# Kernel tuning notes

Measured on AMD Instinct MI355X. Metric: run time of the kernel, lower is better.

The kernel has to match this reference:

```python
import jax, jax.numpy as jnp
import numpy as np
from jax import lax

DIM = 256
HEADS = 8
C3 = DIM * 3 // 4  # 192
C1 = DIM // 4      # 64


def conv1x1(x, w):
    # x: [b,c,h,w], w: [o,c] (1x1 conv, no bias)
    return jnp.einsum('bchw,oc->bohw', x, w)


def dwconv3x3(x, w):
    # x: [b,c,h,w], w: [c,1,3,3] depthwise
    return lax.conv_general_dilated(
        x, w, window_strides=(1, 1), padding='SAME',
        feature_group_count=x.shape[1],
        dimension_numbers=('NCHW', 'OIHW', 'NCHW'))


def l2norm(x, eps=1e-12):
    # torch F.normalize: x / max(||x||, eps) along last dim
    n = jnp.sqrt(jnp.sum(x * x, axis=-1, keepdims=True))
    return x / jnp.maximum(n, eps)


def setup_inputs() -> dict:
    key = jax.random.key(0)
    ks = jax.random.split(key, 10)
    s = 0.02
    return {
        'x': jax.random.normal(ks[0], (4, DIM, 128, 128), jnp.float32),
        'k_v': jax.random.normal(ks[1], (4, 256), jnp.float32),
        'temperature': jnp.ones((HEADS, 1, 1), jnp.float32),
        'w_kR': jax.random.normal(ks[2], (C3, 192), jnp.float32) * s,
        'w_kI': jax.random.normal(ks[3], (C1, 64), jnp.float32) * s,
        'w_qR': jax.random.normal(ks[4], (DIM, C3), jnp.float32) * s,
        'w_qdw': jax.random.normal(ks[5], (DIM, 1, 3, 3), jnp.float32) * s,
        'w_kvI': jax.random.normal(ks[6], (2 * DIM, C1), jnp.float32) * s,
        'w_kvdw': jax.random.normal(ks[7], (2 * DIM, 1, 3, 3), jnp.float32) * s,
        'w_proj': jax.random.normal(ks[8], (DIM, DIM), jnp.float32) * s,
    }


def reference(x, k_v, temperature, w_kR, w_kI, w_qR, w_qdw, w_kvI, w_kvdw, w_proj):
    b, c, h, w = x.shape
    # FiLM-style modulation: x * kv + x
    kvr = (k_v[:, :192] @ w_kR.T)[:, :, None, None]  # [b, C3, 1, 1]
    kvi = (k_v[:, 192:] @ w_kI.T)[:, :, None, None]  # [b, C1, 1, 1]
    x_r = x[:, :C3] * kvr + x[:, :C3]
    x_i = x[:, C3:] * kvi + x[:, C3:]
    # QKV projections
    q = dwconv3x3(conv1x1(x_r, w_qR), w_qdw)          # [b, dim, h, w]
    kv = dwconv3x3(conv1x1(x_i, w_kvI), w_kvdw)       # [b, 2*dim, h, w]
    k, v = jnp.split(kv, 2, axis=1)
    hd = DIM // HEADS
    hw = h * w
    q = q.reshape(b, HEADS, hd, hw)
    k = k.reshape(b, HEADS, hd, hw)
    v = v.reshape(b, HEADS, hd, hw)
    # channel-wise (transposed) attention with L2 norm + temperature
    q = l2norm(q)
    k = l2norm(k)
    attn = jnp.einsum('bhcn,bhdn->bhcd', q, k) * temperature  # [b,H,hd,hd]
    attn = jax.nn.softmax(attn, axis=-1)
    out = jnp.einsum('bhcd,bhdn->bhcn', attn, v)
    out = out.reshape(b, DIM, h, w)
    return conv1x1(out, w_proj)
```

## Files before the change

### kernel.cpp

```cpp
#include <hip/hip_runtime.h>
#include <math.h>

#define HW 16384

typedef unsigned int uint;
typedef short bfrag __attribute__((ext_vector_type(8)));
typedef float f32x4 __attribute__((ext_vector_type(4)));

union FragCvt { uint4 u; bfrag v; };

__device__ inline uint pack2bf(float a, float b) {
  uint ua = __builtin_bit_cast(uint, a);
  uint ub = __builtin_bit_cast(uint, b);
  ua = (ua + 0x7FFFu + ((ua >> 16) & 1u)) >> 16;
  ub = (ub + 0x7FFFu + ((ub >> 16) & 1u)) & 0xFFFF0000u;
  return ua | ub;
}

__device__ inline void cvt_hilo(float4 a, float4 b, bfrag& hi, bfrag& lo) {
  float v0[8] = {a.x, a.y, a.z, a.w, b.x, b.y, b.z, b.w};
  uint hv[4], lv[4];
  #pragma unroll
  for (int i = 0; i < 4; ++i) {
    float x0 = v0[2 * i], x1 = v0[2 * i + 1];
    uint h = pack2bf(x0, x1);
    float h0 = __builtin_bit_cast(float, h << 16);
    float h1 = __builtin_bit_cast(float, h & 0xFFFF0000u);
    hv[i] = h;
    lv[i] = pack2bf(x0 - h0, x1 - h1);
  }
  FragCvt ch, cl;
  ch.u = make_uint4(hv[0], hv[1], hv[2], hv[3]);
  cl.u = make_uint4(lv[0], lv[1], lv[2], lv[3]);
  hi = ch.v;
  lo = cl.v;
}

#define LDS_BARRIER() do { \
  asm volatile("s_waitcnt lgkmcnt(0)" ::: "memory"); \
  __builtin_amdgcn_s_barrier(); \
} while (0)

__global__ __launch_bounds__(256) void mod_kernel(
    const float* __restrict__ kv, const float* __restrict__ wkR,
    const float* __restrict__ wkI, float* __restrict__ mod,
    float* __restrict__ S)
{
  int b = blockIdx.x;
  int c = threadIdx.x;
  float4 z4 = make_float4(0.f, 0.f, 0.f, 0.f);
  float4* sp = (float4*)(S + (((size_t)b * 256 + c) << 5));
  #pragma unroll
  for (int i = 0; i < 8; ++i) sp[i] = z4;

  const float* kvb = kv + b * 256;
  float s = 0.f;
  if (c < 192) {
    const float* wr = wkR + c * 192;
    for (int j = 0; j < 192; ++j) s += kvb[j] * wr[j];
  } else {
    const float* wi = wkI + (c - 192) * 64;
    for (int j = 0; j < 64; ++j) s += kvb[192 + j] * wi[j];
  }
  mod[b * 256 + c] = 1.f + s;
}

__device__ __forceinline__ void mgemm_body(
    const float* __restrict__ Wt, int ldW,
    const float* __restrict__ Xt,
    const float* __restrict__ modc,
    float* __restrict__ Yt,
    int K, int t, unsigned short* Al, unsigned short* Bl, float* Ml)
{
  int w = t >> 6, l = t & 63;
  int wm = (w >> 1) * 64, wn = (w & 1) * 64;
  int lm = l & 15, lk = (l >> 4) * 8;

  int am = t >> 1, ako = (t & 1) * 16;
  int bn = t & 127, bo = (t >> 7) * 8;

  Ml[t] = (modc && t < K) ? modc[t] : 1.f;

  f32x4 acc[4][4];
  #pragma unroll
  for (int fi = 0; fi < 4; ++fi)
    #pragma unroll
    for (int fj = 0; fj < 4; ++fj) acc[fi][fj] = {0.f, 0.f, 0.f, 0.f};

  float xrA[16], xrB[16];
  float4 wv0, wv1, wv2, wv3;

  auto load_x = [&](float* xr, int k0) {
    #pragma unroll
    for (int i = 0; i < 2; ++i) {
      int kb = k0 + bo + i * 16;
      #pragma unroll
      for (int r = 0; r < 8; ++r)
        xr[i * 8 + r] = Xt[(size_t)(kb + r) * HW + bn];
    }
  };
  auto load_w = [&](int k0) {
    const float* wsrc = Wt + (size_t)am * ldW + k0 + ako;
    wv0 = *(const float4*)(wsrc);
    wv1 = *(const float4*)(wsrc + 4);
    wv2 = *(const float4*)(wsrc + 8);
    wv3 = *(const float4*)(wsrc + 12);
  };
  auto pack_a = [&]() {
    uint4 aw0, aw1;
    aw0.x = pack2bf(wv0.x, wv0.y); aw0.y = pack2bf(wv0.z, wv0.w);
    aw0.z = pack2bf(wv1.x, wv1.y); aw0.w = pack2bf(wv1.z, wv1.w);
    aw1.x = pack2bf(wv2.x, wv2.y); aw1.y = pack2bf(wv2.z, wv2.w);
    aw1.z = pack2bf(wv3.x, wv3.y); aw1.w = pack2bf(wv3.z, wv3.w);
    *(uint4*)&Al[am * 40 + ako] = aw0;
    *(uint4*)&Al[am * 40 + ako + 8] = aw1;
  };
  auto pack_b = [&](const float* xr, int k0) {
    #pragma unroll
    for (int i = 0; i < 2; ++i) {
      float4 m0 = *(const float4*)&Ml[k0 + bo + i * 16];
      float4 m1 = *(const float4*)&Ml[k0 + bo + i * 16 + 4];
      uint4 bw;
      bw.x = pack2bf(xr[i * 8 + 0] * m0.x, xr[i * 8 + 1] * m0.y);
      bw.y = pack2bf(xr[i * 8 + 2] * m0.z, xr[i * 8 + 3] * m0.w);
      bw.z = pack2bf(xr[i * 8 + 4] * m1.x, xr[i * 8 + 5] * m1.y);
      bw.w = pack2bf(xr[i * 8 + 6] * m1.z, xr[i * 8 + 7] * m1.w);
      *(uint4*)&Bl[bn * 40 + bo + i * 16] = bw;
    }
  };
  auto mfma_step = [&]() {
    bfrag af[4], bfr[4];
    #pragma unroll
    for (int fj = 0; fj < 4; ++fj) {
      FragCvt cv;
      cv.u = *(const uint4*)&Al[(wm + fj * 16 + lm) * 40 + lk];
      af[fj] = cv.v;
    }
    #pragma unroll
    for (int fi = 0; fi < 4; ++fi) {
      FragCvt cv;
      cv.u = *(const uint4*)&Bl[(wn + fi * 16 + lm) * 40 + lk];
      bfr[fi] = cv.v;
    }
    #pragma unroll
    for (int fi = 0; fi < 4; ++fi)
      #pragma unroll
      for (int fj = 0; fj < 4; ++fj)
        acc[fi][fj] = __builtin_amdgcn_mfma_f32_16x16x32_bf16(
            bfr[fi], af[fj], acc[fi][fj], 0, 0, 0);
  };

  load_x(xrA, 0);
  load_x(xrB, 32);
  load_w(0);

  for (int k0 = 0; k0 < K; k0 += 64) {
    LDS_BARRIER();
    pack_a();
    if (k0 + 32 < K) load_w(k0 + 32);
    pack_b(xrA, k0);
    if (k0 + 64 < K) load_x(xrA, k0 + 64);
    LDS_BARRIER();
    mfma_step();

    LDS_BARRIER();
    pack_a();
    if (k0 + 64 < K) load_w(k0 + 64);
    pack_b(xrB, k0 + 32);
    if (k0 + 96 < K) load_x(xrB, k0 + 96);
    LDS_BARRIER();
    mfma_step();
  }

  int ph = (l >> 4) * 4;
  #pragma unroll
  for (int fi = 0; fi < 4; ++fi)
    #pragma unroll
    for (int fj = 0; fj < 4; ++fj)
      *(f32x4*)&Yt[(size_t)(wm + fj * 16 + lm) * HW + wn + fi * 16 + ph] =
          acc[fi][fj];
}

__global__ __launch_bounds__(256, 2) void mgemm(
    const float* __restrict__ W, int ldW, size_t Wbstride,
    const float* __restrict__ X, int c0, size_t Xbstride,
    const float* __restrict__ mod,
    float* __restrict__ Y, size_t Ybstride, int K)
{
  __shared__ unsigned short Al[128 * 40];
  __shared__ unsigned short Bl[128 * 40];
  __shared__ float Ml[256];
  int b = blockIdx.z, mt = blockIdx.y, nt = blockIdx.x;
  mgemm_body(W + (size_t)b * Wbstride + (size_t)mt * 128 * ldW, ldW,
             X + (size_t)b * Xbstride + (size_t)c0 * HW + nt * 128,
             mod ? mod + b * 256 + c0 : (const float*)nullptr,
             Y + (size_t)b * Ybstride + (size_t)mt * 128 * HW + nt * 128,
             K, threadIdx.x, Al, Bl, Ml);
}

__global__ __launch_bounds__(256, 2) void mgemm_qk(
    const float* __restrict__ wqR, const float* __restrict__ wkvI,
    const float* __restrict__ X, const float* __restrict__ mod,
    float* __restrict__ Yq, float* __restrict__ Yk)
{
  __shared__ unsigned short Al[128 * 40];
  __shared__ unsigned short Bl[128 * 40];
  __shared__ float Ml[256];
  int b = blockIdx.z, mt = blockIdx.y, nt = blockIdx.x;
  if (mt < 2) {
    mgemm_body(wqR + (size_t)mt * 128 * 192, 192,
               X + (size_t)b * 4194304 + nt * 128,
               mod + b * 256,
               Yq + (size_t)b * 4194304 + (size_t)mt * 128 * HW + nt * 128,
               192, threadIdx.x, Al, Bl, Ml);
  } else {
    int m2 = mt - 2;
    mgemm_body(wkvI + (size_t)m2 * 128 * 64, 64,
               X + (size_t)b * 4194304 + (size_t)192 * HW + nt * 128,
               mod + b * 256 + 192,
               Yk + (size_t)b * 4194304 + (size_t)m2 * 128 * HW + nt * 128,
               64, threadIdx.x, Al, Bl, Ml);
  }
}

__global__ __launch_bounds__(256) void dwconv_kernel(
    const float* __restrict__ in, size_t in_bstride,
    const float* __restrict__ wdw,
    float* __restrict__ out, size_t out_bstride,
    float* __restrict__ ssq)
{
  int c = blockIdx.x;
  int b = blockIdx.y;
  int t = threadIdx.x;
  int r = t >> 5;
  int xq = t & 31;

  const float4* ip4 = (const float4*)(in + (size_t)b * in_bstride + ((size_t)c << 14));
  float4* op4 = (float4*)(out + (size_t)b * out_bstride + ((size_t)c << 14));
  const float* wp = wdw + c * 9;
  float w0 = wp[0], w1 = wp[1], w2 = wp[2], w3 = wp[3], w4 = wp[4],
        w5 = wp[5], w6 = wp[6], w7 = wp[7], w8 = wp[8];

  const float4 z4 = make_float4(0.f, 0.f, 0.f, 0.f);
  int y0 = r << 4;

  float4 a = (y0 > 0) ? ip4[((y0 - 1) << 5) + xq] : z4;
  float4 bb = ip4[(y0 << 5) + xq];

  float aL = __shfl_up(a.w, 1);  if (xq == 0)  aL = 0.f;
  float aR = __shfl_down(a.x, 1); if (xq == 31) aR = 0.f;
  float bL = __shfl_up(bb.w, 1); if (xq == 0)  bL = 0.f;
  float bR = __shfl_down(bb.x, 1); if (xq == 31) bR = 0.f;

  float ss = 0.f;
  #pragma unroll
  for (int i = 0; i < 16; ++i) {
    int y = y0 + i;
    int yc = (y + 1 < 128) ? (y + 1) : 127;
    float4 cc = ip4[(yc << 5) + xq];
    if (y + 1 >= 128) { cc.x = 0.f; cc.y = 0.f; cc.z = 0.f; cc.w = 0.f; }
    float cL = __shfl_up(cc.w, 1);  if (xq == 0)  cL = 0.f;
    float cR = __shfl_down(cc.x, 1); if (xq == 31) cR = 0.f;

    float4 o;
    o.x = w0 * aL  + w1 * a.x + w2 * a.y +
          w3 * bL  + w4 * bb.x + w5 * bb.y +
          w6 * cL  + w7 * cc.x + w8 * cc.y;
    o.y = w0 * a.x + w1 * a.y + w2 * a.z +
          w3 * bb.x + w4 * bb.y + w5 * bb.z +
          w6 * cc.x + w7 * cc.y + w8 * cc.z;
    o.z = w0 * a.y + w1 * a.z + w2 * a.w +
          w3 * bb.y + w4 * bb.z + w5 * bb.w +
          w6 * cc.y + w7 * cc.z + w8 * cc.w;
    o.w = w0 * a.z + w1 * a.w + w2 * aR +
          w3 * bb.z + w4 * bb.w + w5 * bR +
          w6 * cc.z + w7 * cc.w + w8 * cR;

    op4[(y << 5) + xq] = o;
    ss += o.x * o.x + o.y * o.y + o.z * o.z + o.w * o.w;

    a = bb; aL = bL; aR = bR;
    bb = cc; bL = cL; bR = cR;
  }

  if (ssq) {
    #pragma unroll
    for (int off = 32; off > 0; off >>= 1) ss += __shfl_down(ss, off);
    __shared__ float red[4];
    if ((t & 63) == 0) red[t >> 6] = ss;
    __syncthreads();
    if (t == 0) ssq[b * 256 + c] = red[0] + red[1] + red[2] + red[3];
  }
}

__global__ __launch_bounds__(256) void gram_kernel(
    const float* __restrict__ qdw, const float* __restrict__ kdw,
    float* __restrict__ S)
{
  int chunk = blockIdx.x, h = blockIdx.y, b = blockIdx.z;
  int t = threadIdx.x;
  int w = t >> 6, l = t & 63;
  int lm = l & 15;
  int lk8 = (l >> 4) * 8;

  const float* qh = qdw + (((size_t)b * 256 + h * 32) << 14);
  const float* kh = kdw + (((size_t)b * 256 + h * 32) << 14);
  const float* q0 = qh + ((size_t)lm << 14);
  const float* q1 = q0 + ((size_t)16 << 14);
  const float* k0 = kh + ((size_t)lm << 14);
  const float* k1 = k0 + ((size_t)16 << 14);

  int px0 = chunk * 1024 + w * 256 + lk8;

  f32x4 acc[2][2], accl[2][2];
  #pragma unroll
  for (int mi = 0; mi < 2; ++mi)
    #pragma unroll
    for (int nj = 0; nj < 2; ++nj) {
      acc[mi][nj] = {0.f, 0.f, 0.f, 0.f};
      accl[mi][nj] = {0.f, 0.f, 0.f, 0.f};
    }

  #pragma unroll 2
  for (int s = 0; s < 8; ++s) {
    int px = px0 + s * 32;
    float4 a0 = *(const float4*)(q0 + px);
    float4 a1 = *(const float4*)(q0 + px + 4);
    float4 a2 = *(const float4*)(q1 + px);
    float4 a3 = *(const float4*)(q1 + px + 4);
    float4 b0 = *(const float4*)(k0 + px);
    float4 b1 = *(const float4*)(k0 + px + 4);
    float4 b2 = *(const float4*)(k1 + px);
    float4 b3 = *(const float4*)(k1 + px + 4);

    bfrag qhF[2], qlF[2], khF[2], klF[2];
    cvt_hilo(a0, a1, qhF[0], qlF[0]);
    cvt_hilo(a2, a3, qhF[1], qlF[1]);
    cvt_hilo(b0, b1, khF[0], klF[0]);
    cvt_hilo(b2, b3, khF[1], klF[1]);

    #pragma unroll
    for (int mi = 0; mi < 2; ++mi)
      #pragma unroll
      for (int nj = 0; nj < 2; ++nj) {
        acc[mi][nj] = __builtin_amdgcn_mfma_f32_16x16x32_bf16(
            qhF[mi], khF[nj], acc[mi][nj], 0, 0, 0);
        accl[mi][nj] = __builtin_amdgcn_mfma_f32_16x16x32_bf16(
            qhF[mi], klF[nj], accl[mi][nj], 0, 0, 0);
        accl[mi][nj] = __builtin_amdgcn_mfma_f32_16x16x32_bf16(
            qlF[mi], khF[nj], accl[mi][nj], 0, 0, 0);
      }
  }

  __shared__ float red[4][1024];
  int orow = (l >> 4) * 4;
  #pragma unroll
  for (int mi = 0; mi < 2; ++mi)
    #pragma unroll
    for (int nj = 0; nj < 2; ++nj)
      #pragma unroll
      for (int r = 0; r < 4; ++r)
        red[w][(mi * 16 + orow + r) * 32 + nj * 16 + lm] =
            acc[mi][nj][r] + accl[mi][nj][r];
  __syncthreads();
  float* Sp = S + (((size_t)b * 8 + h) << 10);
  for (int idx = t; idx < 1024; idx += 256)
    atomicAdd(&Sp[idx], red[0][idx] + red[1][idx] + red[2][idx] + red[3][idx]);
}

__global__ __launch_bounds__(256) void softmax_mbuild(
    const float* __restrict__ S, const float* __restrict__ ssq,
    const float* __restrict__ ssk, const float* __restrict__ temp,
    const float* __restrict__ wproj, float* __restrict__ M)
{
  int o = blockIdx.x, b = blockIdx.y;
  int t = threadIdx.x;
  __shared__ float At[8 * 32 * 33];
  __shared__ float Iq[256], Ik[256], Wp[256];

  Iq[t] = 1.f / fmaxf(sqrtf(ssq[b * 256 + t]), 1e-12f);
  Ik[t] = 1.f / fmaxf(sqrtf(ssk[b * 256 + t]), 1e-12f);
  Wp[t] = wproj[o * 256 + t];
  __syncthreads();

  int h = t >> 5, c = t & 31;
  const float* row = S + (((size_t)b * 8 + h) << 10) + c * 32;
  float invq = Iq[h * 32 + c];
  float T = temp[h];
  float lg[32];
  float mx = -1e30f;
  #pragma unroll
  for (int d = 0; d < 32; ++d) {
    float v = row[d] * invq * Ik[h * 32 + d] * T;
    lg[d] = v;
    mx = fmaxf(mx, v);
  }
  float sum = 0.f;
  #pragma unroll
  for (int d = 0; d < 32; ++d) { float e = expf(lg[d] - mx); lg[d] = e; sum += e; }
  float inv = 1.f / sum;
  float* arow = &At[(h * 32 + c) * 33];
  #pragma unroll
  for (int d = 0; d < 32; ++d) arow[d] = lg[d] * inv;
  __syncthreads();

  int d2 = t & 31, h2 = t >> 5;
  float s = 0.f;
  #pragma unroll
  for (int cc = 0; cc < 32; ++cc)
    s += Wp[h2 * 32 + cc] * At[(h2 * 32 + cc) * 33 + d2];
  M[((size_t)b * 256 + o) * 256 + t] = s;
}

extern "C" void kernel_launch(void* const* d_in, const int* in_sizes, int n_in,
                              void* d_out, int out_size, void* d_ws, size_t ws_size,
                              hipStream_t stream)
{
  const float* x      = (const float*)d_in[0];
  const float* k_v    = (const float*)d_in[1];
  const float* temp   = (const float*)d_in[2];
  const float* w_kR   = (const float*)d_in[3];
  const float* w_kI   = (const float*)d_in[4];
  const float* w_qR   = (const float*)d_in[5];
  const float* w_qdw  = (const float*)d_in[6];
  const float* w_kvI  = (const float*)d_in[7];
  const float* w_kvdw = (const float*)d_in[8];
  const float* w_proj = (const float*)d_in[9];
  float* out = (float*)d_out;

  float* ws   = (float*)d_ws;
  float* bufA = ws;
  float* bufB = ws + 16777216;
  float* bufC = ws + 33554432;
  float* sm   = ws + 50331648;
  float* mod  = sm;
  float* ssq  = sm + 1024;
  float* ssk  = sm + 2048;
  float* S    = sm + 3072;
  float* M    = sm + 3072 + 32768;

  mod_kernel<<<dim3(4), dim3(256), 0, stream>>>(k_v, w_kR, w_kI, mod, S);

  mgemm_qk<<<dim3(128, 4, 4), dim3(256), 0, stream>>>(
      w_qR, w_kvI, x, mod, bufA, bufB);

  dwconv_kernel<<<dim3(256, 4), dim3(256), 0, stream>>>(
      bufB, 4194304, w_kvdw, bufC, 4194304, ssk);

  dwconv_kernel<<<dim3(256, 4), dim3(256), 0, stream>>>(
      bufA, 4194304, w_qdw, bufB, 4194304, ssq);

  gram_kernel<<<dim3(16, 8, 4), dim3(256), 0, stream>>>(bufB, bufC, S);

  mgemm<<<dim3(128, 2, 4), dim3(256), 0, stream>>>(
      w_kvI + 256 * 64, 64, 0, x, 192, 4194304, mod, bufA, 4194304, 64);

  softmax_mbuild<<<dim3(256, 4), dim3(256), 0, stream>>>(
      S, ssq, ssk, temp, w_proj, M);

  dwconv_kernel<<<dim3(256, 4), dim3(256), 0, stream>>>(
      bufA, 4194304, w_kvdw + 256 * 9, bufC, 4194304, (float*)nullptr);

  mgemm<<<dim3(128, 2, 4), dim3(256), 0, stream>>>(
      M, 256, 65536, bufC, 0, 4194304, (const float*)nullptr, out, 4194304, 256);
}
```

Before: 320.0 us.

## Preload full weight tile to LDS and double-buffer activation tiles in 1x1 GEMMs

Adds a new GEMM body that converts the whole 128xK weight slab to bf16 in shared memory once, instead of streaming it per K-step. Activation tiles are double-buffered, with register prefetch of the next chunk, so there are fewer barriers per iteration. It is used for the fused q/kv projection and the v projection through a new mgemm_k64 kernel with higher occupancy bounds. The larger LDS footprint (about 51KB for K=192) may reduce occupancy for the qk kernel.

```diff
diff --git a/kernel.cpp b/kernel.cpp
--- a/kernel.cpp
+++ b/kernel.cpp
@@ -63,6 +63,155 @@
     for (int j = 0; j < 64; ++j) s += kvb[192 + j] * wi[j];
   }
   mod[b * 256 + c] = 1.f + s;
+}
+
+__device__ __forceinline__ void mgemm_body2(
+    const float* __restrict__ Wt,
+    const float* __restrict__ Xt,
+    const float* __restrict__ modc,
+    float* __restrict__ Yt,
+    int K, int Kp, int t,
+    unsigned short* Wl, unsigned short* Bl, float* Ml)
+{
+  int w = t >> 6, l = t & 63;
+  int wm = (w >> 1) * 64, wn = (w & 1) * 64;
+  int lm = l & 15, lk = (l >> 4) * 8;
+  int bn = t & 127, bo = (t >> 7) * 8;
+
+  Ml[t] = (t < K) ? modc[t] : 1.f;
+
+  {
+    int total = 128 * K;
+    for (int base = t * 8; base < total; base += 2048) {
+      int row = base / K;
+      int kk = base - row * K;
+      const float* src = Wt + base;
+      float4 a0 = *(const float4*)(src);
+      float4 a1 = *(const float4*)(src + 4);
+      uint4 pw;
+      pw.x = pack2bf(a0.x, a0.y); pw.y = pack2bf(a0.z, a0.w);
+      pw.z = pack2bf(a1.x, a1.y); pw.w = pack2bf(a1.z, a1.w);
+      *(uint4*)&Wl[row * Kp + kk] = pw;
+    }
+  }
+
+  f32x4 acc[4][4];
+  #pragma unroll
+  for (int fi = 0; fi < 4; ++fi)
+    #pragma unroll
+    for (int fj = 0; fj < 4; ++fj) acc[fi][fj] = {0.f, 0.f, 0.f, 0.f};
+
+  float xrA[16], xrB[16];
+  auto load_x = [&](float* xr, int k0) {
+    #pragma unroll
+    for (int i = 0; i < 2; ++i) {
+      int kb = k0 + bo + i * 16;
+      #pragma unroll
+      for (int r = 0; r < 8; ++r)
+        xr[i * 8 + r] = Xt[(size_t)(kb + r) * HW + bn];
+    }
+  };
+  auto pack_b = [&](const float* xr, int k0, unsigned short* blp) {
+    #pragma unroll
+    for (int i = 0; i < 2; ++i) {
+      float4 m0 = *(const float4*)&Ml[k0 + bo + i * 16];
+      float4 m1 = *(const float4*)&Ml[k0 + bo + i * 16 + 4];
+      uint4 bw;
+      bw.x = pack2bf(xr[i * 8 + 0] * m0.x, xr[i * 8 + 1] * m0.y);
+      bw.y = pack2bf(xr[i * 8 + 2] * m0.z, xr[i * 8 + 3] * m0.w);
+      bw.z = pack2bf(xr[i * 8 + 4] * m1.x, xr[i * 8 + 5] * m1.y);
+      bw.w = pack2bf(xr[i * 8 + 6] * m1.z, xr[i * 8 + 7] * m1.w);
+      *(uint4*)&blp[bn * 40 + bo + i * 16] = bw;
+    }
+  };
+  auto mfma_step = [&](int k0, const unsigned short* blp) {
+    bfrag af[4], bfr[4];
+    #pragma unroll
+    for (int fj = 0; fj < 4; ++fj) {
+      FragCvt cv;
+      cv.u = *(const uint4*)&Wl[(wm + fj * 16 + lm) * Kp + k0 + lk];
+      af[fj] = cv.v;
+    }
+    #pragma unroll
+    for (int fi = 0; fi < 4; ++fi) {
+      FragCvt cv;
+      cv.u = *(const uint4*)&blp[(wn + fi * 16 + lm) * 40 + lk];
+      bfr[fi] = cv.v;
+    }
+    #pragma unroll
+    for (int fi = 0; fi < 4; ++fi)
+      #pragma unroll
+      for (int fj = 0; fj < 4; ++fj)
+        acc[fi][fj] = __builtin_amdgcn_mfma_f32_16x16x32_bf16(
+            bfr[fi], af[fj], acc[fi][fj], 0, 0, 0);
+  };
+
+  load_x(xrA, 0);
+  load_x(xrB, 32);
+
+  LDS_BARRIER();
+
+  unsigned short* bl0 = Bl;
+  unsigned short* bl1 = Bl + 128 * 40;
+  for (int k0 = 0; k0 < K; k0 += 64) {
+    pack_b(xrA, k0, bl0);
+    if (k0 + 64 < K) load_x(xrA, k0 + 64);
+    LDS_BARRIER();
+    mfma_step(k0, bl0);
+
+    pack_b(xrB, k0 + 32, bl1);
+    if (k0 + 96 < K) load_x(xrB, k0 + 96);
+    LDS_BARRIER();
+    mfma_step(k0 + 32, bl1);
+  }
+
+  int ph = (l >> 4) * 4;
+  #pragma unroll
+  for (int fi = 0; fi < 4; ++fi)
+    #pragma unroll
+    for (int fj = 0; fj < 4; ++fj)
+      *(f32x4*)&Yt[(size_t)(wm + fj * 16 + lm) * HW + wn + fi * 16 + ph] =
+          acc[fi][fj];
+}
+
+__global__ __launch_bounds__(256, 2) void mgemm_qk(
+    const float* __restrict__ wqR, const float* __restrict__ wkvI,
+    const float* __restrict__ X, const float* __restrict__ mod,
+    float* __restrict__ Yq, float* __restrict__ Yk)
+{
+  __shared__ unsigned short Wl[128 * 200];
+  __shared__ unsigned short Bl[2 * 128 * 40];
+  __shared__ float Ml[256];
+  int b = blockIdx.z, mt = blockIdx.y, nt = blockIdx.x;
+  if (mt < 2) {
+    mgemm_body2(wqR + (size_t)mt * 128 * 192,
+                X + (size_t)b * 4194304 + nt * 128,
+                mod + b * 256,
+                Yq + (size_t)b * 4194304 + (size_t)mt * 128 * HW + nt * 128,
+                192, 200, threadIdx.x, Wl, Bl, Ml);
+  } else {
+    int m2 = mt - 2;
+    mgemm_body2(wkvI + (size_t)m2 * 128 * 64,
+                X + (size_t)b * 4194304 + (size_t)192 * HW + nt * 128,
+                mod + b * 256 + 192,
+                Yk + (size_t)b * 4194304 + (size_t)m2 * 128 * HW + nt * 128,
+                64, 72, threadIdx.x, Wl, Bl, Ml);
+  }
+}
+
+__global__ __launch_bounds__(256, 4) void mgemm_k64(
+    const float* __restrict__ W, const float* __restrict__ X, int c0,
+    const float* __restrict__ mod, float* __restrict__ Y)
+{
+  __shared__ unsigned short Wl[128 * 72];
+  __shared__ unsigned short Bl[2 * 128 * 40];
+  __shared__ float Ml[256];
+  int b = blockIdx.z, mt = blockIdx.y, nt = blockIdx.x;
+  mgemm_body2(W + (size_t)mt * 128 * 64,
+              X + (size_t)b * 4194304 + (size_t)c0 * HW + nt * 128,
+              mod + b * 256 + c0,
+              Y + (size_t)b * 4194304 + (size_t)mt * 128 * HW + nt * 128,
+              64, 72, threadIdx.x, Wl, Bl, Ml);
 }
 
 __device__ __forceinline__ void mgemm_body(
@@ -196,31 +345,6 @@
              mod ? mod + b * 256 + c0 : (const float*)nullptr,
              Y + (size_t)b * Ybstride + (size_t)mt * 128 * HW + nt * 128,
              K, threadIdx.x, Al, Bl, Ml);
-}
-
-__global__ __launch_bounds__(256, 2) void mgemm_qk(
-    const float* __restrict__ wqR, const float* __restrict__ wkvI,
-    const float* __restrict__ X, const float* __restrict__ mod,
-    float* __restrict__ Yq, float* __restrict__ Yk)
-{
-  __shared__ unsigned short Al[128 * 40];
-  __shared__ unsigned short Bl[128 * 40];
-  __shared__ float Ml[256];
-  int b = blockIdx.z, mt = blockIdx.y, nt = blockIdx.x;
-  if (mt < 2) {
-    mgemm_body(wqR + (size_t)mt * 128 * 192, 192,
-               X + (size_t)b * 4194304 + nt * 128,
-               mod + b * 256,
-               Yq + (size_t)b * 4194304 + (size_t)mt * 128 * HW + nt * 128,
-               192, threadIdx.x, Al, Bl, Ml);
-  } else {
-    int m2 = mt - 2;
-    mgemm_body(wkvI + (size_t)m2 * 128 * 64, 64,
-               X + (size_t)b * 4194304 + (size_t)192 * HW + nt * 128,
-               mod + b * 256 + 192,
-               Yk + (size_t)b * 4194304 + (size_t)m2 * 128 * HW + nt * 128,
-               64, threadIdx.x, Al, Bl, Ml);
-  }
 }
 
 __global__ __launch_bounds__(256) void dwconv_kernel(
@@ -452,8 +576,8 @@
 
   gram_kernel<<<dim3(16, 8, 4), dim3(256), 0, stream>>>(bufB, bufC, S);
 
-  mgemm<<<dim3(128, 2, 4), dim3(256), 0, stream>>>(
-      w_kvI + 256 * 64, 64, 0, x, 192, 4194304, mod, bufA, 4194304, 64);
+  mgemm_k64<<<dim3(128, 2, 4), dim3(256), 0, stream>>>(
+      w_kvI + 256 * 64, x, 192, mod, bufA);
 
   softmax_mbuild<<<dim3(256, 4), dim3(256), 0, stream>>>(
       S, ssq, ssk, temp, w_proj, M);
```

Measured after the change: 319.9 us. Within noise of the previous version (-0.0%).

## Fuse V projection into gram kernel, V dwconv into softmax, store V as bf16

Applied to the files above, without the earlier changes.

The V 1x1 projection GEMM now runs as extra blocks of the gram kernel, and the V depthwise conv runs as extra blocks of the softmax/M-build kernel. This cuts the launch count from five to three and lets independent work overlap. The V dwconv output is stored as bf16, and a new final GEMM reads bf16 directly, which halves that intermediate's write and read traffic. The gram grid gains many idle blocks (mt>=2 return early), and the gram kernel now uses launch_bounds(256,2) with shared LDS.

```diff
diff --git a/kernel.cpp b/kernel.cpp
--- a/kernel.cpp
+++ b/kernel.cpp
@@ -179,23 +179,6 @@
     for (int fj = 0; fj < 4; ++fj)
       *(f32x4*)&Yt[(size_t)(wm + fj * 16 + lm) * HW + wn + fi * 16 + ph] =
           acc[fi][fj];
-}
-
-__global__ __launch_bounds__(256, 2) void mgemm(
-    const float* __restrict__ W, int ldW, size_t Wbstride,
-    const float* __restrict__ X, int c0, size_t Xbstride,
-    const float* __restrict__ mod,
-    float* __restrict__ Y, size_t Ybstride, int K)
-{
-  __shared__ unsigned short Al[128 * 40];
-  __shared__ unsigned short Bl[128 * 40];
-  __shared__ float Ml[256];
-  int b = blockIdx.z, mt = blockIdx.y, nt = blockIdx.x;
-  mgemm_body(W + (size_t)b * Wbstride + (size_t)mt * 128 * ldW, ldW,
-             X + (size_t)b * Xbstride + (size_t)c0 * HW + nt * 128,
-             mod ? mod + b * 256 + c0 : (const float*)nullptr,
-             Y + (size_t)b * Ybstride + (size_t)mt * 128 * HW + nt * 128,
-             K, threadIdx.x, Al, Bl, Ml);
 }
 
 __global__ __launch_bounds__(256, 2) void mgemm_qk(
@@ -293,12 +276,31 @@
   }
 }
 
-__global__ __launch_bounds__(256) void gram_kernel(
+__global__ __launch_bounds__(256, 2) void gram_v_kernel(
     const float* __restrict__ qdw, const float* __restrict__ kdw,
-    float* __restrict__ S)
-{
-  int chunk = blockIdx.x, h = blockIdx.y, b = blockIdx.z;
+    float* __restrict__ S,
+    const float* __restrict__ wv, const float* __restrict__ X,
+    const float* __restrict__ mod, float* __restrict__ Yv)
+{
+  __shared__ __align__(16) unsigned char smem[21504];
   int t = threadIdx.x;
+  int b = blockIdx.z;
+
+  if (blockIdx.x >= 16) {
+    if (blockIdx.y >= 2) return;
+    int nt = blockIdx.x - 16, mt = blockIdx.y;
+    unsigned short* Al = (unsigned short*)smem;
+    unsigned short* Bl = Al + 128 * 40;
+    float* Ml = (float*)(smem + 20480);
+    mgemm_body(wv + (size_t)mt * 128 * 64, 64,
+               X + (size_t)b * 4194304 + (size_t)192 * HW + nt * 128,
+               mod + b * 256 + 192,
+               Yv + (size_t)b * 4194304 + (size_t)mt * 128 * HW + nt * 128,
+               64, t, Al, Bl, Ml);
+    return;
+  }
+
+  int chunk = blockIdx.x, h = blockIdx.y;
   int w = t >> 6, l = t & 63;
   int lm = l & 15;
   int lk8 = (l >> 4) * 8;
@@ -352,7 +354,7 @@
       }
   }
 
-  __shared__ float red[4][1024];
+  float* red = (float*)smem;
   int orow = (l >> 4) * 4;
   #pragma unroll
   for (int mi = 0; mi < 2; ++mi)
@@ -360,21 +362,75 @@
     for (int nj = 0; nj < 2; ++nj)
       #pragma unroll
       for (int r = 0; r < 4; ++r)
-        red[w][(mi * 16 + orow + r) * 32 + nj * 16 + lm] =
+        red[w * 1024 + (mi * 16 + orow + r) * 32 + nj * 16 + lm] =
             acc[mi][nj][r] + accl[mi][nj][r];
   __syncthreads();
   float* Sp = S + (((size_t)b * 8 + h) << 10);
   for (int idx = t; idx < 1024; idx += 256)
-    atomicAdd(&Sp[idx], red[0][idx] + red[1][idx] + red[2][idx] + red[3][idx]);
-}
-
-__global__ __launch_bounds__(256) void softmax_mbuild(
+    atomicAdd(&Sp[idx],
+              red[idx] + red[1024 + idx] + red[2048 + idx] + red[3072 + idx]);
+}
+
+__global__ __launch_bounds__(256) void smb_vdw_kernel(
     const float* __restrict__ S, const float* __restrict__ ssq,
     const float* __restrict__ ssk, const float* __restrict__ temp,
-    const float* __restrict__ wproj, float* __restrict__ M)
-{
-  int o = blockIdx.x, b = blockIdx.y;
+    const float* __restrict__ wproj, float* __restrict__ M,
+    const float* __restrict__ vpre, const float* __restrict__ wvdw,
+    unsigned short* __restrict__ vdw)
+{
   int t = threadIdx.x;
+  int b = blockIdx.y;
+
+  if (blockIdx.x >= 256) {
+    int c = blockIdx.x - 256;
+    int r = t >> 5;
+    int xq = t & 31;
+    const float4* ip4 =
+        (const float4*)(vpre + (size_t)b * 4194304 + ((size_t)c << 14));
+    uint2* op2 = (uint2*)(vdw + (size_t)b * 4194304 + ((size_t)c << 14));
+    const float* wp = wvdw + c * 9;
+    float w0 = wp[0], w1 = wp[1], w2 = wp[2], w3 = wp[3], w4 = wp[4],
+          w5 = wp[5], w6 = wp[6], w7 = wp[7], w8 = wp[8];
+    const float4 z4 = make_float4(0.f, 0.f, 0.f, 0.f);
+    int y0 = r << 4;
+    float4 a = (y0 > 0) ? ip4[((y0 - 1) << 5) + xq] : z4;
+    float4 bb = ip4[(y0 << 5) + xq];
+    float aL = __shfl_up(a.w, 1);  if (xq == 0)  aL = 0.f;
+    float aR = __shfl_down(a.x, 1); if (xq == 31) aR = 0.f;
+    float bL = __shfl_up(bb.w, 1); if (xq == 0)  bL = 0.f;
+    float bR = __shfl_down(bb.x, 1); if (xq == 31) bR = 0.f;
+    #pragma unroll
+    for (int i = 0; i < 16; ++i) {
+      int y = y0 + i;
+      int yc = (y + 1 < 128) ? (y + 1) : 127;
+      float4 cc = ip4[(yc << 5) + xq];
+      if (y + 1 >= 128) { cc.x = 0.f; cc.y = 0.f; cc.z = 0.f; cc.w = 0.f; }
+      float cL = __shfl_up(cc.w, 1);  if (xq == 0)  cL = 0.f;
+      float cR = __shfl_down(cc.x, 1); if (xq == 31) cR = 0.f;
+      float4 o;
+      o.x = w0 * aL  + w1 * a.x + w2 * a.y +
+            w3 * bL  + w4 * bb.x + w5 * bb.y +
+            w6 * cL  + w7 * cc.x + w8 * cc.y;
+      o.y = w0 * a.x + w1 * a.y + w2 * a.z +
+            w3 * bb.x + w4 * bb.y + w5 * bb.z +
+            w6 * cc.x + w7 * cc.y + w8 * cc.z;
+      o.z = w0 * a.y + w1 * a.z + w2 * a.w +
+            w3 * bb.y + w4 * bb.z + w5 * bb.w +
+            w6 * cc.y + w7 * cc.z + w8 * cc.w;
+      o.w = w0 * a.z + w1 * a.w + w2 * aR +
+            w3 * bb.z + w4 * bb.w + w5 * bR +
+            w6 * cc.z + w7 * cc.w + w8 * cR;
+      uint2 ob;
+      ob.x = pack2bf(o.x, o.y);
+      ob.y = pack2bf(o.z, o.w);
+      op2[(y << 5) + xq] = ob;
+      a = bb; aL = bL; aR = bR;
+      bb = cc; bL = cL; bR = cR;
+    }
+    return;
+  }
+
+  int o = blockIdx.x;
   __shared__ float At[8 * 32 * 33];
   __shared__ float Iq[256], Ik[256], Wp[256];
 
@@ -410,6 +466,123 @@
   for (int cc = 0; cc < 32; ++cc)
     s += Wp[h2 * 32 + cc] * At[(h2 * 32 + cc) * 33 + d2];
   M[((size_t)b * 256 + o) * 256 + t] = s;
+}
+
+__global__ __launch_bounds__(256, 2) void mgemm_bx(
+    const float* __restrict__ Mw, const unsigned short* __restrict__ Xb,
+    float* __restrict__ out)
+{
+  __shared__ unsigned short Al[128 * 40];
+  __shared__ unsigned short Bl[128 * 40];
+  int b = blockIdx.z, mt = blockIdx.y, nt = blockIdx.x;
+  const float* Wt = Mw + (size_t)b * 65536 + (size_t)mt * 128 * 256;
+  const unsigned short* Xt = Xb + (size_t)b * 4194304 + nt * 128;
+  float* Yt = out + (size_t)b * 4194304 + (size_t)mt * 128 * HW + nt * 128;
+  int t = threadIdx.x;
+  const int K = 256;
+
+  int w = t >> 6, l = t & 63;
+  int wm = (w >> 1) * 64, wn = (w & 1) * 64;
+  int lm = l & 15, lk = (l >> 4) * 8;
+  int am = t >> 1, ako = (t & 1) * 16;
+  int bn = t & 127, bo = (t >> 7) * 8;
+
+  f32x4 acc[4][4];
+  #pragma unroll
+  for (int fi = 0; fi < 4; ++fi)
+    #pragma unroll
+    for (int fj = 0; fj < 4; ++fj) acc[fi][fj] = {0.f, 0.f, 0.f, 0.f};
+
+  unsigned short xrA[16], xrB[16];
+  float4 wv0, wv1, wv2, wv3;
+
+  auto load_x = [&](unsigned short* xr, int k0) {
+    #pragma unroll
+    for (int i = 0; i < 2; ++i) {
+      int kb = k0 + bo + i * 16;
+      #pragma unroll
+      for (int r = 0; r < 8; ++r)
+        xr[i * 8 + r] = Xt[(size_t)(kb + r) * HW + bn];
+    }
+  };
+  auto load_w = [&](int k0) {
+    const float* wsrc = Wt + (size_t)am * 256 + k0 + ako;
+    wv0 = *(const float4*)(wsrc);
+    wv1 = *(const float4*)(wsrc + 4);
+    wv2 = *(const float4*)(wsrc + 8);
+    wv3 = *(const float4*)(wsrc + 12);
+  };
+  auto pack_a = [&]() {
+    uint4 aw0, aw1;
+    aw0.x = pack2bf(wv0.x, wv0.y); aw0.y = pack2bf(wv0.z, wv0.w);
+    aw0.z = pack2bf(wv1.x, wv1.y); aw0.w = pack2bf(wv1.z, wv1.w);
+    aw1.x = pack2bf(wv2.x, wv2.y); aw1.y = pack2bf(wv2.z, wv2.w);
+    aw1.z = pack2bf(wv3.x, wv3.y); aw1.w = pack2bf(wv3.z, wv3.w);
+    *(uint4*)&Al[am * 40 + ako] = aw0;
+    *(uint4*)&Al[am * 40 + ako + 8] = aw1;
+  };
+  auto pack_b = [&](const unsigned short* xr) {
+    #pragma unroll
+    for (int i = 0; i < 2; ++i) {
+      uint4 bw;
+      bw.x = (uint)xr[i * 8 + 0] | ((uint)xr[i * 8 + 1] << 16);
+      bw.y = (uint)xr[i * 8 + 2] | ((uint)xr[i * 8 + 3] << 16);
+      bw.z = (uint)xr[i * 8 + 4] | ((uint)xr[i * 8 + 5] << 16);
+      bw.w = (uint)xr[i * 8 + 6] | ((uint)xr[i * 8 + 7] << 16);
+      *(uint4*)&Bl[bn * 40 + bo + i * 16] = bw;
+    }
+  };
+  auto mfma_step = [&]() {
+    bfrag af[4], bfr[4];
+    #pragma unroll
+    for (int fj = 0; fj < 4; ++fj) {
+      FragCvt cv;
+      cv.u = *(const uint4*)&Al[(wm + fj * 16 + lm) * 40 + lk];
+      af[fj] = cv.v;
+    }
+    #pragma unroll
+    for (int fi = 0; fi < 4; ++fi) {
+      FragCvt cv;
+      cv.u = *(const uint4*)&Bl[(wn + fi * 16 + lm) * 40 + lk];
+      bfr[fi] = cv.v;
+    }
+    #pragma unroll
+    for (int fi = 0; fi < 4; ++fi)
+      #pragma unroll
+      for (int fj = 0; fj < 4; ++fj)
+        acc[fi][fj] = __builtin_amdgcn_mfma_f32_16x16x32_bf16(
+            bfr[fi], af[fj], acc[fi][fj], 0, 0, 0);
+  };
+
+  load_x(xrA, 0);
+  load_x(xrB, 32);
+  load_w(0);
+
+  for (int k0 = 0; k0 < K; k0 += 64) {
+    LDS_BARRIER();
+    pack_a();
+    if (k0 + 32 < K) load_w(k0 + 32);
+    pack_b(xrA);
+    if (k0 + 64 < K) load_x(xrA, k0 + 64);
+    LDS_BARRIER();
+    mfma_step();
+
+    LDS_BARRIER();
+    pack_a();
+    if (k0 + 64 < K) load_w(k0 + 64);
+    pack_b(xrB);
+    if (k0 + 96 < K) load_x(xrB, k0 + 96);
+    LDS_BARRIER();
+    mfma_step();
+  }
+
+  int ph = (l >> 4) * 4;
+  #pragma unroll
+  for (int fi = 0; fi < 4; ++fi)
+    #pragma unroll
+    for (int fj = 0; fj < 4; ++fj)
+      *(f32x4*)&Yt[(size_t)(wm + fj * 16 + lm) * HW + wn + fi * 16 + ph] =
+          acc[fi][fj];
 }
 
 extern "C" void kernel_launch(void* const* d_in, const int* in_sizes, int n_in,
@@ -450,17 +623,13 @@
   dwconv_kernel<<<dim3(256, 4), dim3(256), 0, stream>>>(
       bufA, 4194304, w_qdw, bufB, 4194304, ssq);
 
-  gram_kernel<<<dim3(16, 8, 4), dim3(256), 0, stream>>>(bufB, bufC, S);
-
-  mgemm<<<dim3(128, 2, 4), dim3(256), 0, stream>>>(
-      w_kvI + 256 * 64, 64, 0, x, 192, 4194304, mod, bufA, 4194304, 64);
-
-  softmax_mbuild<<<dim3(256, 4), dim3(256), 0, stream>>>(
-      S, ssq, ssk, temp, w_proj, M);
-
-  dwconv_kernel<<<dim3(256, 4), dim3(256), 0, stream>>>(
-      bufA, 4194304, w_kvdw + 256 * 9, bufC, 4194304, (float*)nullptr);
-
-  mgemm<<<dim3(128, 2, 4), dim3(256), 0, stream>>>(
-      M, 256, 65536, bufC, 0, 4194304, (const float*)nullptr, out, 4194304, 256);
-}
+  gram_v_kernel<<<dim3(144, 8, 4), dim3(256), 0, stream>>>(
+      bufB, bufC, S, w_kvI + 256 * 64, x, mod, bufA);
+
+  smb_vdw_kernel<<<dim3(512, 4), dim3(256), 0, stream>>>(
+      S, ssq, ssk, temp, w_proj, M,
+      bufA, w_kvdw + 256 * 9, (unsigned short*)bufC);
+
+  mgemm_bx<<<dim3(128, 2, 4), dim3(256), 0, stream>>>(
+      M, (const unsigned short*)bufC, out);
+}
```

Measured after the change: 304.2 us. -4.9%, faster.
